# Kernel optimization log

Hardware: AMD Instinct MI355X
Metric: run time of the kernel (lower is better)

Reference implementation:

```python
import jax, jax.numpy as jnp
import numpy as np

B, T, D_IN, D_OUT, N_HEAD = 2, 2048, 1024, 1024, 16
HEAD_DIM = D_OUT // N_HEAD


def setup_inputs() -> dict:
    key = jax.random.key(0)
    k1, k2, k3, k4 = jax.random.split(key, 4)
    s = 0.02  # init scale for weights
    return {
        "x": jax.random.normal(k1, (B, T, D_IN), jnp.float32),
        "Wq": jax.random.normal(k2, (D_OUT, D_IN), jnp.float32) * s,
        "Wk": jax.random.normal(k3, (D_OUT, D_IN), jnp.float32) * s,
        "Wv": jax.random.normal(k4, (D_OUT, D_IN), jnp.float32) * s,
    }


def reference(x, Wq, Wk, Wv):
    b, t, _ = x.shape
    h, hd = N_HEAD, HEAD_DIM
    # Linear projections (torch Linear: x @ W.T), split heads -> [b,h,t,hd]
    q = (x @ Wq.T).reshape(b, t, h, hd).transpose(0, 2, 1, 3)
    k = (x @ Wk.T).reshape(b, t, h, hd).transpose(0, 2, 1, 3)
    v = (x @ Wv.T).reshape(b, t, h, hd).transpose(0, 2, 1, 3)
    # raw scores [b,h,t,t], causal mask BEFORE scaling (as in source)
    omega = jnp.einsum("bhqd,bhkd->bhqk", q, k)
    causal = jnp.triu(jnp.ones((t, t), dtype=bool), k=1)
    omega = jnp.where(causal, -jnp.inf, omega)
    attw = jax.nn.softmax(omega / jnp.sqrt(jnp.asarray(hd, omega.dtype)), axis=-1)
    ctx = jnp.einsum("bhqk,bhkd->bhqd", attw, v)  # [b,h,t,hd]
    # Faithful to source: transpose(2,3) then view(B,T,d_out)
    out = jnp.swapaxes(ctx, 2, 3).reshape(b, t, D_OUT)
    return out
```

## Files before the change

kernel.cpp:

```cpp
#include <hip/hip_runtime.h>
#include <stdint.h>

typedef __attribute__((ext_vector_type(8))) short s16x8;
typedef __attribute__((ext_vector_type(4))) float f32x4;

#define T_   2048
#define NH   16
#define HD   64
#define DIN  1024
#define LS   72

__device__ __forceinline__ unsigned short f2bf(float f) {
  union { float f; uint32_t u; } c; c.f = f;
  uint32_t u = c.u;
  return (unsigned short)((u + 0x7FFFu + ((u >> 16) & 1u)) >> 16);
}

#define GLL(gp, lp) __builtin_amdgcn_global_load_lds( \
    (__attribute__((address_space(1))) void*)(gp),    \
    (__attribute__((address_space(3))) void*)(lp), 16, 0, 0)

__global__ __launch_bounds__(256) void cvt_kernel(
    const float* __restrict__ x,  const float* __restrict__ wq,
    const float* __restrict__ wk, const float* __restrict__ wv,
    unsigned short* __restrict__ xb, unsigned short* __restrict__ wb) {
  int i = (blockIdx.x * 256 + threadIdx.x) * 4;
  float4 v;
  unsigned short* dp;
  if (i < 4194304) {
    v = *(const float4*)(x + i);
    dp = xb + i;
  } else {
    int j = i - 4194304;
    int seg = j >> 20, r = j & 1048575;
    const float* w = (seg == 0) ? wq : (seg == 1) ? wk : wv;
    v = *(const float4*)(w + r);
    dp = wb + j;
  }
  ushort4 o;
  o.x = f2bf(v.x); o.y = f2bf(v.y); o.z = f2bf(v.z); o.w = f2bf(v.w);
  *(ushort4*)dp = o;
}

__global__ __launch_bounds__(256) void qkv_gemm(
    const unsigned short* __restrict__ A, const unsigned short* __restrict__ Bm,
    unsigned short* __restrict__ qkv) {
  __shared__ __attribute__((aligned(16))) unsigned short Alds[128 * 64];
  __shared__ __attribute__((aligned(16))) unsigned short Blds[128 * 64];
  const int tid = threadIdx.x;
  const int lane = tid & 63, wave = tid >> 6;
  const int wm = wave >> 1, wn = wave & 1;
  const int m0 = blockIdx.y * 128, n0 = blockIdx.x * 128;

  f32x4 acc[4][4] = {};

  const int srow = wave * 32 + (lane >> 3);
  const int scol = (((lane & 7) ^ ((lane >> 3) & 7))) * 8;
  const unsigned short* ag = A  + (size_t)(m0 + srow) * DIN + scol;
  const unsigned short* bg = Bm + (size_t)(n0 + srow) * DIN + scol;
  unsigned short* al = &Alds[wave * 32 * 64];
  unsigned short* bl = &Blds[wave * 32 * 64];

  const int l16 = lane & 15, quad = lane >> 4;
  const int sw = l16 & 7;

  for (int k0 = 0; k0 < DIN; k0 += 64) {
    __syncthreads();
#pragma unroll
    for (int i = 0; i < 4; i++) {
      GLL(ag + (size_t)i * 8 * DIN + k0, al + i * 512);
      GLL(bg + (size_t)i * 8 * DIN + k0, bl + i * 512);
    }
    __syncthreads();
#pragma unroll
    for (int ks = 0; ks < 2; ks++) {
      const int cl = ((ks * 4 + quad) ^ sw) * 8;
      s16x8 af[4], bf[4];
#pragma unroll
      for (int mt = 0; mt < 4; mt++)
        af[mt] = *(const s16x8*)&Alds[(wm * 64 + mt * 16 + l16) * 64 + cl];
#pragma unroll
      for (int nt = 0; nt < 4; nt++)
        bf[nt] = *(const s16x8*)&Blds[(wn * 64 + nt * 16 + l16) * 64 + cl];
#pragma unroll
      for (int mt = 0; mt < 4; mt++)
#pragma unroll
        for (int nt = 0; nt < 4; nt++)
          acc[mt][nt] = __builtin_amdgcn_mfma_f32_16x16x32_bf16(af[mt], bf[nt], acc[mt][nt], 0, 0, 0);
    }
  }

#pragma unroll
  for (int mt = 0; mt < 4; mt++) {
    int mbase = m0 + wm * 64 + mt * 16 + (quad << 2);
    int b = mbase >> 11, t = mbase & 2047;
#pragma unroll
    for (int nt = 0; nt < 4; nt++) {
      int n = n0 + wn * 64 + nt * 16 + l16;
      int sel = n >> 10, h = (n >> 6) & 15, d = n & 63;
      int bh = b * NH + h;
      if (sel == 2) {
        ushort4 pk;
        pk.x = f2bf(acc[mt][nt][0]); pk.y = f2bf(acc[mt][nt][1]);
        pk.z = f2bf(acc[mt][nt][2]); pk.w = f2bf(acc[mt][nt][3]);
        *(ushort4*)&qkv[8388608 + (size_t)(bh * HD + d) * T_ + t] = pk;
      } else {
#pragma unroll
        for (int r = 0; r < 4; r++)
          qkv[(size_t)sel * 4194304 + (size_t)(bh * T_ + t + r) * HD + d] =
              f2bf(acc[mt][nt][r]);
      }
    }
  }
}

__global__ __launch_bounds__(256) void attn_kernel(
    const unsigned short* __restrict__ qkv, float* __restrict__ out) {
  __shared__ __attribute__((aligned(16))) unsigned short Klds[64 * LS];
  __shared__ __attribute__((aligned(16))) unsigned short Vt[64 * LS];
  __shared__ __attribute__((aligned(16))) unsigned short Plds[4 * 16 * LS];

  const int lane = threadIdx.x & 63, wave = threadIdx.x >> 6;
  const int l16 = lane & 15, quad = lane >> 4;
  const int qt = 31 - blockIdx.y, bh = blockIdx.x;
  const int q0 = qt * 64;
  const size_t bh_off = (size_t)bh * (T_ * HD);
  const unsigned short* Q  = qkv;
  const unsigned short* Kb = qkv + 4194304 + bh_off;
  const unsigned short* Vb = qkv + 8388608 + bh_off;

  s16x8 qf[2];
  {
    const unsigned short* qp =
        Q + bh_off + (size_t)(q0 + wave * 16 + l16) * HD + quad * 8;
    qf[0] = *(const s16x8*)(qp);
    qf[1] = *(const s16x8*)(qp + 32);
  }

  const int sr = threadIdx.x >> 3;
  const int sc = (threadIdx.x & 7) * 8;

  s16x8 kr0 = *(const s16x8*)&Kb[(size_t)sr * HD + sc];
  s16x8 kr1 = *(const s16x8*)&Kb[(size_t)(sr + 32) * HD + sc];
  s16x8 vr0 = *(const s16x8*)&Vb[(size_t)sr * T_ + sc];
  s16x8 vr1 = *(const s16x8*)&Vb[(size_t)(sr + 32) * T_ + sc];

  const float scale_log2 = 0.18033688011112042f;
  float lsum = 0.f;
  f32x4 o[4] = {};
  unsigned short* pw = &Plds[wave * 16 * LS];

  for (int kt = 0; kt <= qt; kt++) {
    __syncthreads();
    *(s16x8*)&Klds[sr * LS + sc] = kr0;
    *(s16x8*)&Klds[(sr + 32) * LS + sc] = kr1;
    *(s16x8*)&Vt[sr * LS + sc] = vr0;
    *(s16x8*)&Vt[(sr + 32) * LS + sc] = vr1;
    if (kt < qt) {
      const unsigned short* kp = Kb + (size_t)(kt + 1) * 64 * HD;
      const unsigned short* vp = Vb + (kt + 1) * 64;
      kr0 = *(const s16x8*)&kp[(size_t)sr * HD + sc];
      kr1 = *(const s16x8*)&kp[(size_t)(sr + 32) * HD + sc];
      vr0 = *(const s16x8*)&vp[(size_t)sr * T_ + sc];
      vr1 = *(const s16x8*)&vp[(size_t)(sr + 32) * T_ + sc];
    }
    __syncthreads();

    f32x4 s[4] = {};
#pragma unroll
    for (int kk = 0; kk < 2; kk++)
#pragma unroll
      for (int nt = 0; nt < 4; nt++) {
        s16x8 kf = *(const s16x8*)&Klds[(nt * 16 + l16) * LS + kk * 32 + quad * 8];
        s[nt] = __builtin_amdgcn_mfma_f32_16x16x32_bf16(kf, qf[kk], s[nt], 0, 0, 0);
      }

    const int lim = (kt == qt) ? (wave * 16 + l16) : 1000;
#pragma unroll
    for (int nt = 0; nt < 4; nt++) {
      ushort4 pk;
      float p0, p1, p2, p3;
      const int kb = nt * 16 + quad * 4;
      p0 = (kb + 0 <= lim) ? exp2f(s[nt][0] * scale_log2) : 0.f;
      p1 = (kb + 1 <= lim) ? exp2f(s[nt][1] * scale_log2) : 0.f;
      p2 = (kb + 2 <= lim) ? exp2f(s[nt][2] * scale_log2) : 0.f;
      p3 = (kb + 3 <= lim) ? exp2f(s[nt][3] * scale_log2) : 0.f;
      lsum += (p0 + p1) + (p2 + p3);
      pk.x = f2bf(p0); pk.y = f2bf(p1); pk.z = f2bf(p2); pk.w = f2bf(p3);
      *(ushort4*)&pw[l16 * LS + nt * 16 + quad * 4] = pk;
    }

#pragma unroll
    for (int kk = 0; kk < 2; kk++) {
      s16x8 pf = *(const s16x8*)&pw[l16 * LS + kk * 32 + quad * 8];
#pragma unroll
      for (int dt = 0; dt < 4; dt++) {
        s16x8 vf = *(const s16x8*)&Vt[(dt * 16 + l16) * LS + kk * 32 + quad * 8];
        o[dt] = __builtin_amdgcn_mfma_f32_16x16x32_bf16(pf, vf, o[dt], 0, 0, 0);
      }
    }
  }

  lsum += __shfl_xor(lsum, 16);
  lsum += __shfl_xor(lsum, 32);
  float linv = 1.f / lsum;
  float li[4];
#pragma unroll
  for (int r = 0; r < 4; r++) li[r] = __shfl(linv, quad * 4 + r);

#pragma unroll
  for (int dt = 0; dt < 4; dt++) {
    float4 v = make_float4(o[dt][0] * li[0], o[dt][1] * li[1],
                           o[dt][2] * li[2], o[dt][3] * li[3]);
    *(float4*)(out + (size_t)bh * (HD * T_) + (size_t)(dt * 16 + l16) * T_ +
               q0 + wave * 16 + quad * 4) = v;
  }
}

extern "C" void kernel_launch(void* const* d_in, const int* in_sizes, int n_in,
                              void* d_out, int out_size, void* d_ws, size_t ws_size,
                              hipStream_t stream) {
  const float* x  = (const float*)d_in[0];
  const float* wq = (const float*)d_in[1];
  const float* wk = (const float*)d_in[2];
  const float* wv = (const float*)d_in[3];
  float* out = (float*)d_out;

  unsigned short* xb  = (unsigned short*)d_ws;
  unsigned short* wb  = xb + 4194304;
  unsigned short* qkv = wb + 3145728;

  cvt_kernel<<<7168, 256, 0, stream>>>(x, wq, wk, wv, xb, wb);
  dim3 g1(24, 32);
  qkv_gemm<<<g1, 256, 0, stream>>>(xb, wb, qkv);
  dim3 g2(32, 32);
  attn_kernel<<<g2, 256, 0, stream>>>(qkv, out);
}
```

Baseline: 161.5 us.

## Double query tile per attention block, fold scale into Q, MFMA row sums

```diff
diff --git a/kernel.cpp b/kernel.cpp
--- a/kernel.cpp
+++ b/kernel.cpp
@@ -1,4 +1,5 @@
 #include <hip/hip_runtime.h>
+#include <hip/hip_bf16.h>
 #include <stdint.h>
 
 typedef __attribute__((ext_vector_type(8))) short s16x8;
@@ -9,11 +10,17 @@
 #define HD   64
 #define DIN  1024
 #define LS   72
+#define SCALE_LOG2 0.18033688011112042f
 
 __device__ __forceinline__ unsigned short f2bf(float f) {
   union { float f; uint32_t u; } c; c.f = f;
   uint32_t u = c.u;
   return (unsigned short)((u + 0x7FFFu + ((u >> 16) & 1u)) >> 16);
+}
+
+__device__ __forceinline__ uint32_t pk_bf16(float a, float b) {
+  __hip_bfloat162 h = __float22bfloat162_rn(make_float2(a, b));
+  return *reinterpret_cast<uint32_t*>(&h);
 }
 
 #define GLL(gp, lp) __builtin_amdgcn_global_load_lds( \
@@ -105,10 +112,11 @@
         pk.z = f2bf(acc[mt][nt][2]); pk.w = f2bf(acc[mt][nt][3]);
         *(ushort4*)&qkv[8388608 + (size_t)(bh * HD + d) * T_ + t] = pk;
       } else {
+        float qs = (sel == 0) ? SCALE_LOG2 : 1.f;
 #pragma unroll
         for (int r = 0; r < 4; r++)
           qkv[(size_t)sel * 4194304 + (size_t)(bh * T_ + t + r) * HD + d] =
-              f2bf(acc[mt][nt][r]);
+              f2bf(acc[mt][nt][r] * qs);
       }
     }
   }
@@ -118,23 +126,24 @@
     const unsigned short* __restrict__ qkv, float* __restrict__ out) {
   __shared__ __attribute__((aligned(16))) unsigned short Klds[64 * LS];
   __shared__ __attribute__((aligned(16))) unsigned short Vt[64 * LS];
-  __shared__ __attribute__((aligned(16))) unsigned short Plds[4 * 16 * LS];
+  __shared__ __attribute__((aligned(16))) unsigned short Plds[4 * 32 * LS];
 
   const int lane = threadIdx.x & 63, wave = threadIdx.x >> 6;
   const int l16 = lane & 15, quad = lane >> 4;
-  const int qt = 31 - blockIdx.y, bh = blockIdx.x;
-  const int q0 = qt * 64;
+  const int qt = 15 - blockIdx.y, bh = blockIdx.x;
+  const int q0 = qt * 128;
   const size_t bh_off = (size_t)bh * (T_ * HD);
   const unsigned short* Q  = qkv;
   const unsigned short* Kb = qkv + 4194304 + bh_off;
   const unsigned short* Vb = qkv + 8388608 + bh_off;
 
-  s16x8 qf[2];
-  {
+  s16x8 qf[2][2];
+#pragma unroll
+  for (int qtile = 0; qtile < 2; qtile++) {
     const unsigned short* qp =
-        Q + bh_off + (size_t)(q0 + wave * 16 + l16) * HD + quad * 8;
-    qf[0] = *(const s16x8*)(qp);
-    qf[1] = *(const s16x8*)(qp + 32);
+        Q + bh_off + (size_t)(q0 + wave * 32 + qtile * 16 + l16) * HD + quad * 8;
+    qf[qtile][0] = *(const s16x8*)(qp);
+    qf[qtile][1] = *(const s16x8*)(qp + 32);
   }
 
   const int sr = threadIdx.x >> 3;
@@ -145,18 +154,21 @@
   s16x8 vr0 = *(const s16x8*)&Vb[(size_t)sr * T_ + sc];
   s16x8 vr1 = *(const s16x8*)&Vb[(size_t)(sr + 32) * T_ + sc];
 
-  const float scale_log2 = 0.18033688011112042f;
-  float lsum = 0.f;
-  f32x4 o[4] = {};
-  unsigned short* pw = &Plds[wave * 16 * LS];
-
-  for (int kt = 0; kt <= qt; kt++) {
+  const s16x8 onesf = {0x3F80, 0x3F80, 0x3F80, 0x3F80,
+                       0x3F80, 0x3F80, 0x3F80, 0x3F80};
+  f32x4 o[2][4] = {};
+  f32x4 lacc[2] = {};
+
+  const int ktmax = 2 * qt + 1;
+  const int myktmax = (q0 + wave * 32 + 31) >> 6;
+
+  for (int kt = 0; kt <= ktmax; kt++) {
     __syncthreads();
     *(s16x8*)&Klds[sr * LS + sc] = kr0;
     *(s16x8*)&Klds[(sr + 32) * LS + sc] = kr1;
     *(s16x8*)&Vt[sr * LS + sc] = vr0;
     *(s16x8*)&Vt[(sr + 32) * LS + sc] = vr1;
-    if (kt < qt) {
+    if (kt < ktmax) {
       const unsigned short* kp = Kb + (size_t)(kt + 1) * 64 * HD;
       const unsigned short* vp = Vb + (kt + 1) * 64;
       kr0 = *(const s16x8*)&kp[(size_t)sr * HD + sc];
@@ -166,54 +178,77 @@
     }
     __syncthreads();
 
-    f32x4 s[4] = {};
+    if (kt > myktmax) continue;
+
+    f32x4 s[2][4] = {};
 #pragma unroll
     for (int kk = 0; kk < 2; kk++)
 #pragma unroll
       for (int nt = 0; nt < 4; nt++) {
         s16x8 kf = *(const s16x8*)&Klds[(nt * 16 + l16) * LS + kk * 32 + quad * 8];
-        s[nt] = __builtin_amdgcn_mfma_f32_16x16x32_bf16(kf, qf[kk], s[nt], 0, 0, 0);
-      }
-
-    const int lim = (kt == qt) ? (wave * 16 + l16) : 1000;
-#pragma unroll
-    for (int nt = 0; nt < 4; nt++) {
-      ushort4 pk;
-      float p0, p1, p2, p3;
-      const int kb = nt * 16 + quad * 4;
-      p0 = (kb + 0 <= lim) ? exp2f(s[nt][0] * scale_log2) : 0.f;
-      p1 = (kb + 1 <= lim) ? exp2f(s[nt][1] * scale_log2) : 0.f;
-      p2 = (kb + 2 <= lim) ? exp2f(s[nt][2] * scale_log2) : 0.f;
-      p3 = (kb + 3 <= lim) ? exp2f(s[nt][3] * scale_log2) : 0.f;
-      lsum += (p0 + p1) + (p2 + p3);
-      pk.x = f2bf(p0); pk.y = f2bf(p1); pk.z = f2bf(p2); pk.w = f2bf(p3);
-      *(ushort4*)&pw[l16 * LS + nt * 16 + quad * 4] = pk;
+        s[0][nt] = __builtin_amdgcn_mfma_f32_16x16x32_bf16(kf, qf[0][kk], s[0][nt], 0, 0, 0);
+        s[1][nt] = __builtin_amdgcn_mfma_f32_16x16x32_bf16(kf, qf[1][kk], s[1][nt], 0, 0, 0);
+      }
+
+#pragma unroll
+    for (int qtile = 0; qtile < 2; qtile++) {
+      const int qmin = q0 + wave * 32 + qtile * 16;
+      uint32_t* prow = (uint32_t*)&Plds[(wave * 32 + qtile * 16 + l16) * LS];
+      if (kt * 64 + 63 <= qmin) {
+#pragma unroll
+        for (int nt = 0; nt < 4; nt++) {
+          float p0 = exp2f(s[qtile][nt][0]);
+          float p1 = exp2f(s[qtile][nt][1]);
+          float p2 = exp2f(s[qtile][nt][2]);
+          float p3 = exp2f(s[qtile][nt][3]);
+          *(uint2*)&prow[nt * 8 + quad * 2] =
+              make_uint2(pk_bf16(p0, p1), pk_bf16(p2, p3));
+        }
+      } else {
+        const int lim = qmin + l16 - kt * 64;
+#pragma unroll
+        for (int nt = 0; nt < 4; nt++) {
+          const int kb = nt * 16 + quad * 4;
+          float p0 = (kb + 0 <= lim) ? exp2f(s[qtile][nt][0]) : 0.f;
+          float p1 = (kb + 1 <= lim) ? exp2f(s[qtile][nt][1]) : 0.f;
+          float p2 = (kb + 2 <= lim) ? exp2f(s[qtile][nt][2]) : 0.f;
+          float p3 = (kb + 3 <= lim) ? exp2f(s[qtile][nt][3]) : 0.f;
+          *(uint2*)&prow[nt * 8 + quad * 2] =
+              make_uint2(pk_bf16(p0, p1), pk_bf16(p2, p3));
+        }
+      }
     }
 
 #pragma unroll
     for (int kk = 0; kk < 2; kk++) {
-      s16x8 pf = *(const s16x8*)&pw[l16 * LS + kk * 32 + quad * 8];
+      s16x8 pf[2];
+#pragma unroll
+      for (int qtile = 0; qtile < 2; qtile++)
+        pf[qtile] = *(const s16x8*)&Plds[(wave * 32 + qtile * 16 + l16) * LS +
+                                         kk * 32 + quad * 8];
+      lacc[0] = __builtin_amdgcn_mfma_f32_16x16x32_bf16(pf[0], onesf, lacc[0], 0, 0, 0);
+      lacc[1] = __builtin_amdgcn_mfma_f32_16x16x32_bf16(pf[1], onesf, lacc[1], 0, 0, 0);
 #pragma unroll
       for (int dt = 0; dt < 4; dt++) {
         s16x8 vf = *(const s16x8*)&Vt[(dt * 16 + l16) * LS + kk * 32 + quad * 8];
-        o[dt] = __builtin_amdgcn_mfma_f32_16x16x32_bf16(pf, vf, o[dt], 0, 0, 0);
-      }
-    }
-  }
-
-  lsum += __shfl_xor(lsum, 16);
-  lsum += __shfl_xor(lsum, 32);
-  float linv = 1.f / lsum;
-  float li[4];
-#pragma unroll
-  for (int r = 0; r < 4; r++) li[r] = __shfl(linv, quad * 4 + r);
-
-#pragma unroll
-  for (int dt = 0; dt < 4; dt++) {
-    float4 v = make_float4(o[dt][0] * li[0], o[dt][1] * li[1],
-                           o[dt][2] * li[2], o[dt][3] * li[3]);
-    *(float4*)(out + (size_t)bh * (HD * T_) + (size_t)(dt * 16 + l16) * T_ +
-               q0 + wave * 16 + quad * 4) = v;
+        o[0][dt] = __builtin_amdgcn_mfma_f32_16x16x32_bf16(pf[0], vf, o[0][dt], 0, 0, 0);
+        o[1][dt] = __builtin_amdgcn_mfma_f32_16x16x32_bf16(pf[1], vf, o[1][dt], 0, 0, 0);
+      }
+    }
+  }
+
+#pragma unroll
+  for (int qtile = 0; qtile < 2; qtile++) {
+    f32x4 inv;
+#pragma unroll
+    for (int r = 0; r < 4; r++) inv[r] = 1.f / lacc[qtile][r];
+#pragma unroll
+    for (int dt = 0; dt < 4; dt++) {
+      float4 v = make_float4(o[qtile][dt][0] * inv[0], o[qtile][dt][1] * inv[1],
+                             o[qtile][dt][2] * inv[2], o[qtile][dt][3] * inv[3]);
+      *(float4*)(out + (size_t)bh * (HD * T_) + (size_t)(dt * 16 + l16) * T_ +
+                 q0 + wave * 32 + qtile * 16 + quad * 4) = v;
+    }
   }
 }
 
@@ -233,6 +268,6 @@
   cvt_kernel<<<7168, 256, 0, stream>>>(x, wq, wk, wv, xb, wb);
   dim3 g1(24, 32);
   qkv_gemm<<<g1, 256, 0, stream>>>(xb, wb, qkv);
-  dim3 g2(32, 32);
+  dim3 g2(32, 16);
   attn_kernel<<<g2, 256, 0, stream>>>(qkv, out);
 }
```

Result: slower. 172.6 us (+6.9%).

## Fold softmax scale into Q, compute row sums via MFMA, split masked tile

Applied to the files above, without the earlier changes.

```diff
diff --git a/kernel.cpp b/kernel.cpp
--- a/kernel.cpp
+++ b/kernel.cpp
@@ -1,4 +1,5 @@
 #include <hip/hip_runtime.h>
+#include <hip/hip_bf16.h>
 #include <stdint.h>
 
 typedef __attribute__((ext_vector_type(8))) short s16x8;
@@ -8,12 +9,18 @@
 #define NH   16
 #define HD   64
 #define DIN  1024
-#define LS   72
+#define LS   68
+#define SCALE_LOG2 0.18033688011112042f
 
 __device__ __forceinline__ unsigned short f2bf(float f) {
   union { float f; uint32_t u; } c; c.f = f;
   uint32_t u = c.u;
   return (unsigned short)((u + 0x7FFFu + ((u >> 16) & 1u)) >> 16);
+}
+
+__device__ __forceinline__ uint32_t pk_bf16(float a, float b) {
+  __hip_bfloat162 h = __float22bfloat162_rn(make_float2(a, b));
+  return *reinterpret_cast<uint32_t*>(&h);
 }
 
 #define GLL(gp, lp) __builtin_amdgcn_global_load_lds( \
@@ -105,10 +112,11 @@
         pk.z = f2bf(acc[mt][nt][2]); pk.w = f2bf(acc[mt][nt][3]);
         *(ushort4*)&qkv[8388608 + (size_t)(bh * HD + d) * T_ + t] = pk;
       } else {
+        float qs = (sel == 0) ? SCALE_LOG2 : 1.f;
 #pragma unroll
         for (int r = 0; r < 4; r++)
           qkv[(size_t)sel * 4194304 + (size_t)(bh * T_ + t + r) * HD + d] =
-              f2bf(acc[mt][nt][r]);
+              f2bf(acc[mt][nt][r] * qs);
       }
     }
   }
@@ -116,9 +124,9 @@
 
 __global__ __launch_bounds__(256) void attn_kernel(
     const unsigned short* __restrict__ qkv, float* __restrict__ out) {
-  __shared__ __attribute__((aligned(16))) unsigned short Klds[64 * LS];
-  __shared__ __attribute__((aligned(16))) unsigned short Vt[64 * LS];
-  __shared__ __attribute__((aligned(16))) unsigned short Plds[4 * 16 * LS];
+  __shared__ unsigned short Klds[64 * LS];
+  __shared__ unsigned short Vt[64 * LS];
+  __shared__ unsigned short Plds[4 * 16 * LS];
 
   const int lane = threadIdx.x & 63, wave = threadIdx.x >> 6;
   const int l16 = lane & 15, quad = lane >> 4;
@@ -145,9 +153,10 @@
   s16x8 vr0 = *(const s16x8*)&Vb[(size_t)sr * T_ + sc];
   s16x8 vr1 = *(const s16x8*)&Vb[(size_t)(sr + 32) * T_ + sc];
 
-  const float scale_log2 = 0.18033688011112042f;
-  float lsum = 0.f;
+  const s16x8 onesf = {0x3F80, 0x3F80, 0x3F80, 0x3F80,
+                       0x3F80, 0x3F80, 0x3F80, 0x3F80};
   f32x4 o[4] = {};
+  f32x4 lacc = {};
   unsigned short* pw = &Plds[wave * 16 * LS];
 
   for (int kt = 0; kt <= qt; kt++) {
@@ -175,24 +184,35 @@
         s[nt] = __builtin_amdgcn_mfma_f32_16x16x32_bf16(kf, qf[kk], s[nt], 0, 0, 0);
       }
 
-    const int lim = (kt == qt) ? (wave * 16 + l16) : 1000;
-#pragma unroll
-    for (int nt = 0; nt < 4; nt++) {
-      ushort4 pk;
-      float p0, p1, p2, p3;
-      const int kb = nt * 16 + quad * 4;
-      p0 = (kb + 0 <= lim) ? exp2f(s[nt][0] * scale_log2) : 0.f;
-      p1 = (kb + 1 <= lim) ? exp2f(s[nt][1] * scale_log2) : 0.f;
-      p2 = (kb + 2 <= lim) ? exp2f(s[nt][2] * scale_log2) : 0.f;
-      p3 = (kb + 3 <= lim) ? exp2f(s[nt][3] * scale_log2) : 0.f;
-      lsum += (p0 + p1) + (p2 + p3);
-      pk.x = f2bf(p0); pk.y = f2bf(p1); pk.z = f2bf(p2); pk.w = f2bf(p3);
-      *(ushort4*)&pw[l16 * LS + nt * 16 + quad * 4] = pk;
+    uint32_t* prow = (uint32_t*)&Plds[(wave * 16 + l16) * LS];
+    if (kt < qt) {
+#pragma unroll
+      for (int nt = 0; nt < 4; nt++) {
+        float p0 = exp2f(s[nt][0]);
+        float p1 = exp2f(s[nt][1]);
+        float p2 = exp2f(s[nt][2]);
+        float p3 = exp2f(s[nt][3]);
+        *(uint2*)&prow[nt * 8 + quad * 2] =
+            make_uint2(pk_bf16(p0, p1), pk_bf16(p2, p3));
+      }
+    } else {
+      const int lim = wave * 16 + l16;
+#pragma unroll
+      for (int nt = 0; nt < 4; nt++) {
+        const int kb = nt * 16 + quad * 4;
+        float p0 = (kb + 0 <= lim) ? exp2f(s[nt][0]) : 0.f;
+        float p1 = (kb + 1 <= lim) ? exp2f(s[nt][1]) : 0.f;
+        float p2 = (kb + 2 <= lim) ? exp2f(s[nt][2]) : 0.f;
+        float p3 = (kb + 3 <= lim) ? exp2f(s[nt][3]) : 0.f;
+        *(uint2*)&prow[nt * 8 + quad * 2] =
+            make_uint2(pk_bf16(p0, p1), pk_bf16(p2, p3));
+      }
     }
 
 #pragma unroll
     for (int kk = 0; kk < 2; kk++) {
       s16x8 pf = *(const s16x8*)&pw[l16 * LS + kk * 32 + quad * 8];
+      lacc = __builtin_amdgcn_mfma_f32_16x16x32_bf16(pf, onesf, lacc, 0, 0, 0);
 #pragma unroll
       for (int dt = 0; dt < 4; dt++) {
         s16x8 vf = *(const s16x8*)&Vt[(dt * 16 + l16) * LS + kk * 32 + quad * 8];
@@ -201,17 +221,13 @@
     }
   }
 
-  lsum += __shfl_xor(lsum, 16);
-  lsum += __shfl_xor(lsum, 32);
-  float linv = 1.f / lsum;
-  float li[4];
-#pragma unroll
-  for (int r = 0; r < 4; r++) li[r] = __shfl(linv, quad * 4 + r);
-
+  f32x4 inv;
+#pragma unroll
+  for (int r = 0; r < 4; r++) inv[r] = 1.f / lacc[r];
 #pragma unroll
   for (int dt = 0; dt < 4; dt++) {
-    float4 v = make_float4(o[dt][0] * li[0], o[dt][1] * li[1],
-                           o[dt][2] * li[2], o[dt][3] * li[3]);
+    float4 v = make_float4(o[dt][0] * inv[0], o[dt][1] * inv[1],
+                           o[dt][2] * inv[2], o[dt][3] * inv[3]);
     *(float4*)(out + (size_t)bh * (HD * T_) + (size_t)(dt * 16 + l16) * T_ +
                q0 + wave * 16 + quad * 4) = v;
   }
```

Measured after the change: 168.2 us. +4.2%, slower.
